# Performance work log

Hardware: AMD Instinct MI355X
Metric: run time of the kernel (lower is better)

## Reference

```python
import jax, jax.numpy as jnp
import numpy as np

NEG_SLOPE = 0.2


def setup_inputs() -> dict:
    key = jax.random.key(0)
    k1, k2, k3, k4 = jax.random.split(key, 4)
    N, E, IN, OUT = 100000, 1600000, 256, 64
    x = jax.random.normal(k1, (N, IN), dtype=jnp.float32)
    edge_index = jax.random.randint(k2, (2, E), 0, N, dtype=jnp.int64)
    W = jax.random.normal(k3, (IN, OUT), dtype=jnp.float32) * (1.0 / np.sqrt(IN))
    a = jax.random.normal(k4, (2 * OUT,), dtype=jnp.float32) * 0.02
    return {"x": x, "W": W, "a": a, "edge_index": edge_index, "num_nodes": N}


def reference(x, W, a, edge_index, num_nodes):
    # h = W(x): torch Linear without bias == x @ W (W stored as [in_dim, out_dim])
    h = x @ W                                   # [N, out_dim]
    src, dst = edge_index[0], edge_index[1]     # [E], [E]
    out_dim = h.shape[1]
    # e = LeakyReLU(cat([hs, hd]) @ a) == LeakyReLU(hs @ a[:d] + hd @ a[d:])
    s_src = h @ a[:out_dim]                     # [N] per-node src score
    s_dst = h @ a[out_dim:]                     # [N] per-node dst score
    e = jax.nn.leaky_relu(s_src[src] + s_dst[dst], NEG_SLOPE)  # [E]
    # per-destination segment softmax (numerically stable)
    m = jax.ops.segment_max(e, dst, num_segments=num_nodes)   # [N]
    ex = jnp.exp(e - m[dst])                                   # [E]
    denom = jax.ops.segment_sum(ex, dst, num_segments=num_nodes)  # [N]
    alpha = ex / denom[dst]                                    # [E]
    # weighted scatter-sum of source features into destinations
    out = jax.ops.segment_sum(h[src] * alpha[:, None], dst, num_segments=num_nodes)
    return out
```

## Files before the change

### kernel.cpp

```cpp
#include <hip/hip_runtime.h>
#include <hip/hip_bf16.h>
#include <math.h>

#define IN_DIM 256
#define OUT_DIM 64
#define NEG_SLOPE 0.2f
#define LCOLS 80
#define NBMAX 392
#define ECAP  10240
#define SENT  0xFFFFFFFFu
#define SCAP  2560

typedef __attribute__((ext_vector_type(8))) short bf16x8;
typedef __attribute__((ext_vector_type(4))) float f32x4;

static __device__ __forceinline__ ushort f2bf(float f) {
    union { __hip_bfloat16 b; ushort u; } cv;
    cv.b = __float2bfloat16(f);
    return cv.u;
}
static __device__ __forceinline__ float bf2f(ushort u) {
    union { ushort u2[2]; float f; } cv;
    cv.u2[0] = 0; cv.u2[1] = u;
    return cv.f;
}

__global__ __launch_bounds__(1024) void k0_fused(
        const float* __restrict__ W, const float* __restrict__ a,
        ushort* __restrict__ wb, int* __restrict__ gtail)
{
    __shared__ float wa_l[2 * IN_DIM];
    const int tid = threadIdx.x;

    if (tid < 512) gtail[tid] = 0;

    if (tid < IN_DIM) {
        const float* wr = W + (size_t)tid * OUT_DIM;
        float ss = 0.f, sd = 0.f;
        #pragma unroll
        for (int j = 0; j < OUT_DIM; ++j) {
            const float w = wr[j];
            ss = fmaf(w, a[j], ss);
            sd = fmaf(w, a[OUT_DIM + j], sd);
        }
        wa_l[tid] = ss;
        wa_l[IN_DIM + tid] = sd;
    }
    __syncthreads();

    for (int idx = tid; idx < 8 * 4 * LCOLS * 8; idx += 1024) {
        const int j   = idx & 7;
        const int col = (idx >> 3) % LCOLS;
        const int tk  = (idx >> 3) / LCOLS;
        const int k   = (tk >> 2) * 32 + (tk & 3) * 8 + j;
        float v = 0.f;
        if (col < OUT_DIM)           v = W[(size_t)k * OUT_DIM + col];
        else if (col == OUT_DIM)     v = wa_l[k];
        else if (col == OUT_DIM + 1) v = wa_l[IN_DIM + k];
        wb[idx] = f2bf(v);
    }
}

__global__ __launch_bounds__(256) void k1_mfma(
        const float* __restrict__ x, const ushort* __restrict__ wb,
        ushort* __restrict__ hb, float* __restrict__ s_src,
        float* __restrict__ s_dst, int N, int ngroups)
{
    __shared__ f32x4 red[5][4][64];

    const int tid  = threadIdx.x;
    const int wv   = tid >> 6;
    const int lane = tid & 63;
    const int l15  = lane & 15;
    const int khi  = lane >> 4;

    bf16x8 bfrag[2][5];
    #pragma unroll
    for (int tt = 0; tt < 2; ++tt) {
        const int t = 2 * wv + tt;
        #pragma unroll
        for (int c = 0; c < 5; ++c)
            bfrag[tt][c] =
                ((const bf16x8*)wb)[(t * 4 + khi) * LCOLS + c * 16 + l15];
    }

    for (int g = blockIdx.x; g < ngroups; g += gridDim.x) {
        const int row = min(g * 16 + l15, N - 1);
        const float* xp = x + (size_t)row * IN_DIM + wv * 64 + khi * 8;

        const float4 lo0 = *(const float4*)(xp);
        const float4 hi0 = *(const float4*)(xp + 4);
        const float4 lo1 = *(const float4*)(xp + 32);
        const float4 hi1 = *(const float4*)(xp + 36);

        union { bf16x8 v; ushort u[8]; } a0, a1;
        a0.u[0] = f2bf(lo0.x); a0.u[1] = f2bf(lo0.y);
        a0.u[2] = f2bf(lo0.z); a0.u[3] = f2bf(lo0.w);
        a0.u[4] = f2bf(hi0.x); a0.u[5] = f2bf(hi0.y);
        a0.u[6] = f2bf(hi0.z); a0.u[7] = f2bf(hi0.w);
        a1.u[0] = f2bf(lo1.x); a1.u[1] = f2bf(lo1.y);
        a1.u[2] = f2bf(lo1.z); a1.u[3] = f2bf(lo1.w);
        a1.u[4] = f2bf(hi1.x); a1.u[5] = f2bf(hi1.y);
        a1.u[6] = f2bf(hi1.z); a1.u[7] = f2bf(hi1.w);

        f32x4 acc[5] = {{0,0,0,0},{0,0,0,0},{0,0,0,0},{0,0,0,0},{0,0,0,0}};
        #pragma unroll
        for (int c = 0; c < 5; ++c)
            acc[c] = __builtin_amdgcn_mfma_f32_16x16x32_bf16(
                         a0.v, bfrag[0][c], acc[c], 0, 0, 0);
        #pragma unroll
        for (int c = 0; c < 5; ++c)
            acc[c] = __builtin_amdgcn_mfma_f32_16x16x32_bf16(
                         a1.v, bfrag[1][c], acc[c], 0, 0, 0);

        #pragma unroll
        for (int c = 0; c < 5; ++c)
            red[c][wv][lane] = acc[c];
        __syncthreads();

        f32x4 s = red[wv][0][lane];
        #pragma unroll
        for (int sw = 1; sw < 4; ++sw) s += red[wv][sw][lane];

        const int nrow0 = g * 16 + khi * 4;
        #pragma unroll
        for (int r = 0; r < 4; ++r) {
            const int nrow = nrow0 + r;
            if (nrow < N)
                hb[(size_t)nrow * OUT_DIM + wv * 16 + l15] = f2bf(s[r]);
        }

        if (wv == 0) {
            f32x4 s4 = red[4][0][lane];
            #pragma unroll
            for (int sw = 1; sw < 4; ++sw) s4 += red[4][sw][lane];
            #pragma unroll
            for (int r = 0; r < 4; ++r) {
                const int nrow = nrow0 + r;
                if (nrow < N) {
                    if (l15 == 0) s_src[nrow] = s4[r];
                    if (l15 == 1) s_dst[nrow] = s4[r];
                }
            }
        }
        __syncthreads();
    }
}

__global__ __launch_bounds__(256) void kA_bin(
        const int* __restrict__ ei, int* __restrict__ gtail,
        unsigned int* __restrict__ ebuf, int E, int nbuck)
{
    __shared__ unsigned int lbuf[NBMAX][32];
    __shared__ int lcnt[NBMAX];
    __shared__ int lfl[NBMAX];

    const int tid = threadIdx.x;
    for (int r = tid; r < nbuck; r += 256) { lcnt[r] = 0; lfl[r] = 0; }
    __syncthreads();

    const int e0 = (int)(((long long)blockIdx.x * E) / gridDim.x);
    const int e1 = (int)(((long long)(blockIdx.x + 1) * E) / gridDim.x);

    for (int b = e0; b < e1; b += 256) {
        const int i = b + tid;
        if (i < e1) {
            const unsigned int src = (unsigned int)ei[i];
            const int dst = ei[E + i];
            const int c = dst >> 8;
            const int pos = atomicAdd(&lcnt[c], 1);
            lbuf[c][pos & 31] = src | ((unsigned int)(dst & 255) << 17);
        }
        __syncthreads();
        for (int r = tid; r < nbuck; r += 256) {
            int cnt = lcnt[r];
            int fl  = lfl[r];
            while (cnt - fl >= 16) {
                const int gb = atomicAdd(&gtail[r], 16);
                if (gb + 16 <= ECAP) {
                    uint4* dp = (uint4*)(ebuf + (size_t)r * ECAP + gb);
                    const uint4* sp = (const uint4*)&lbuf[r][fl & 31];
                    dp[0] = sp[0]; dp[1] = sp[1]; dp[2] = sp[2]; dp[3] = sp[3];
                }
                fl += 16;
            }
            lfl[r] = fl;
        }
        __syncthreads();
    }

    for (int r = tid; r < nbuck; r += 256) {
        const int cnt = lcnt[r];
        const int fl  = lfl[r];
        if (cnt > fl) {
            const int gb = atomicAdd(&gtail[r], 16);
            if (gb + 16 <= ECAP) {
                unsigned int tmp[16];
                #pragma unroll
                for (int k = 0; k < 16; ++k)
                    tmp[k] = (fl + k < cnt) ? lbuf[r][(fl + k) & 31] : SENT;
                uint4* dp = (uint4*)(ebuf + (size_t)r * ECAP + gb);
                #pragma unroll
                for (int k = 0; k < 4; ++k)
                    dp[k] = make_uint4(tmp[4*k], tmp[4*k+1], tmp[4*k+2], tmp[4*k+3]);
            }
        }
    }
}

__global__ __launch_bounds__(256) void k2_bucket(
        const unsigned int* __restrict__ ebuf, const int* __restrict__ gtail,
        const ushort* __restrict__ hb, const float* __restrict__ s_src,
        const float* __restrict__ s_dst, float* __restrict__ out,
        int N, int nbuck)
{
    __shared__ int hist[64], bse[64], cur[64];
    __shared__ float sdl[64];
    __shared__ int2 spair[SCAP];

    const int bid = blockIdx.x;
    const int xcd = bid & 7;
    const int j8  = bid >> 3;
    const int H   = j8 & 3;
    const int B   = xcd + 8 * (j8 >> 2);
    if (B >= nbuck) return;

    const int tid = threadIdx.x;
    const int slots = min(gtail[B], ECAP);
    const unsigned int* eb = ebuf + (size_t)B * ECAP;
    const int dgb = B * 256 + H * 64;

    if (tid < 64) {
        hist[tid] = 0;
        const int dg = dgb + tid;
        sdl[tid] = (dg < N) ? s_dst[dg] : 0.f;
    }
    __syncthreads();

    for (int i = tid; i < slots; i += 256) {
        const unsigned int e = eb[i];
        if (e != SENT) {
            const int dl = (int)((e >> 17) & 255);
            if ((dl >> 6) == H) atomicAdd(&hist[dl & 63], 1);
        }
    }
    __syncthreads();

    if (tid < 64) {
        const int v = hist[tid];
        int s = v;
        #pragma unroll
        for (int off = 1; off < 64; off <<= 1) {
            const int u = __shfl_up(s, off, 64);
            if (tid >= off) s += u;
        }
        bse[tid] = s - v;
        cur[tid] = s - v;
    }
    __syncthreads();

    for (int i = tid; i < slots; i += 256) {
        const unsigned int e = eb[i];
        if (e != SENT) {
            const int dl = (int)((e >> 17) & 255);
            if ((dl >> 6) == H) {
                const int src = (int)(e & 0x1FFFF);
                const int d   = dl & 63;
                float sc = s_src[src] + sdl[d];
                sc = (sc > 0.f) ? sc : NEG_SLOPE * sc;
                const int pos = atomicAdd(&cur[d], 1);
                if (pos < SCAP)
                    spair[pos] = make_int2(src, __float_as_int(__expf(sc)));
            }
        }
    }
    __syncthreads();

    const int l15 = tid & 15;
    const int qw  = tid >> 4;
    #pragma unroll
    for (int k = 0; k < 4; ++k) {
        const int d  = qw + 16 * k;
        const int dg = dgb + d;
        if (dg >= N) continue;
        const int beg = bse[d];
        const int cnt = hist[d];
        const int je0 = min(beg, SCAP);
        const int je1 = min(beg + cnt, SCAP);
        const int m   = je1 - je0;

        float a0 = 0.f, a1 = 0.f, a2 = 0.f, a3 = 0.f, den = 0.f;
        #pragma unroll 4
        for (int j = 0; j < m; ++j) {
            const int2 p = spair[je0 + j];
            const float ex = __int_as_float(p.y);
            den += ex;
            const ushort4 hv = *(const ushort4*)(hb + ((size_t)p.x << 6) + (l15 << 2));
            a0 = fmaf(ex, bf2f(hv.x), a0);
            a1 = fmaf(ex, bf2f(hv.y), a1);
            a2 = fmaf(ex, bf2f(hv.z), a2);
            a3 = fmaf(ex, bf2f(hv.w), a3);
        }
        const float r = (m > 0) ? 1.f / den : 0.f;
        float4 v;
        v.x = a0 * r; v.y = a1 * r; v.z = a2 * r; v.w = a3 * r;
        *(float4*)(out + ((size_t)dg << 6) + (l15 << 2)) = v;
    }
}

extern "C" void kernel_launch(void* const* d_in, const int* in_sizes, int n_in,
                              void* d_out, int out_size, void* d_ws, size_t ws_size,
                              hipStream_t stream)
{
    const float* x  = (const float*)d_in[0];
    const float* W  = (const float*)d_in[1];
    const float* a  = (const float*)d_in[2];
    const int*   ei = (const int*)d_in[3];

    const int N = in_sizes[0] / IN_DIM;
    const int E = in_sizes[3] / 2;

    float* out = (float*)d_out;

    char* ws = (char*)d_ws;
    ushort* hb     = (ushort*)ws;                  ws += (size_t)N * OUT_DIM * 2;
    float*  s_src  = (float*)ws;                   ws += (size_t)N * 4;
    float*  s_dst  = (float*)ws;                   ws += (size_t)N * 4;
    ushort* wb     = (ushort*)ws;                  ws += 8 * 4 * LCOLS * 8 * 2;
    int*    gtail  = (int*)ws;                     ws += 512 * 4;
    unsigned int* ebuf = (unsigned int*)ws;        ws += (size_t)NBMAX * ECAP * 4;

    const int nbuck = (N + 255) >> 8;

    k0_fused<<<1, 1024, 0, stream>>>(W, a, wb, gtail);

    kA_bin<<<512, 256, 0, stream>>>(ei, gtail, ebuf, E, nbuck);

    const int ngroups = (N + 15) / 16;
    k1_mfma<<<1024, 256, 0, stream>>>(x, wb, hb, s_src, s_dst, N, ngroups);

    const int k2grid = 8 * 4 * ((nbuck + 7) / 8);
    k2_bucket<<<k2grid, 256, 0, stream>>>(ebuf, gtail, hb, s_src, s_dst, out, N, nbuck);
}
```

Baseline: 113.3 us.

## Merge edge binning and MFMA projection into one heterogeneous kernel launch

Combines the edge-binning kernel and the MFMA feature projection kernel into a single launch, with the first 512 blocks doing binning and the remaining 1024 blocks doing the matmul. The two phases are independent, so they can now run concurrently on the GPU and one launch plus its inter-kernel gap disappears. In exchange, every block reserves dynamic LDS sized for the larger binning buffer (about 53 KB), which may lower occupancy for the matmul blocks.

```diff
diff --git a/kernel.cpp b/kernel.cpp
--- a/kernel.cpp
+++ b/kernel.cpp
@@ -10,6 +10,8 @@
 #define ECAP  10240
 #define SENT  0xFFFFFFFFu
 #define SCAP  2560
+#define NBIN  512
+#define KAB_LDS (NBMAX * 32 * 4 + NBMAX * 4 + NBMAX * 4)
 
 typedef __attribute__((ext_vector_type(8))) short bf16x8;
 typedef __attribute__((ext_vector_type(4))) float f32x4;
@@ -61,149 +63,151 @@
     }
 }
 
-__global__ __launch_bounds__(256) void k1_mfma(
+__global__ __launch_bounds__(256) void kAB(
+        const int* __restrict__ ei, int* __restrict__ gtail,
+        unsigned int* __restrict__ ebuf, int E, int nbuck,
         const float* __restrict__ x, const ushort* __restrict__ wb,
         ushort* __restrict__ hb, float* __restrict__ s_src,
         float* __restrict__ s_dst, int N, int ngroups)
 {
-    __shared__ f32x4 red[5][4][64];
-
-    const int tid  = threadIdx.x;
-    const int wv   = tid >> 6;
-    const int lane = tid & 63;
-    const int l15  = lane & 15;
-    const int khi  = lane >> 4;
-
-    bf16x8 bfrag[2][5];
-    #pragma unroll
-    for (int tt = 0; tt < 2; ++tt) {
-        const int t = 2 * wv + tt;
+    extern __shared__ char smem[];
+    const int tid = threadIdx.x;
+
+    if (blockIdx.x < NBIN) {
+        unsigned int (*lbuf)[32] = (unsigned int(*)[32])smem;
+        int* lcnt = (int*)(smem + NBMAX * 32 * 4);
+        int* lfl  = lcnt + NBMAX;
+
+        for (int r = tid; r < nbuck; r += 256) { lcnt[r] = 0; lfl[r] = 0; }
+        __syncthreads();
+
+        const int e0 = (int)(((long long)blockIdx.x * E) / NBIN);
+        const int e1 = (int)(((long long)(blockIdx.x + 1) * E) / NBIN);
+
+        for (int b = e0; b < e1; b += 256) {
+            const int i = b + tid;
+            if (i < e1) {
+                const unsigned int src = (unsigned int)ei[i];
+                const int dst = ei[E + i];
+                const int c = dst >> 8;
+                const int pos = atomicAdd(&lcnt[c], 1);
+                lbuf[c][pos & 31] = src | ((unsigned int)(dst & 255) << 17);
+            }
+            __syncthreads();
+            for (int r = tid; r < nbuck; r += 256) {
+                int cnt = lcnt[r];
+                int fl  = lfl[r];
+                while (cnt - fl >= 16) {
+                    const int gb = atomicAdd(&gtail[r], 16);
+                    if (gb + 16 <= ECAP) {
+                        uint4* dp = (uint4*)(ebuf + (size_t)r * ECAP + gb);
+                        const uint4* sp = (const uint4*)&lbuf[r][fl & 31];
+                        dp[0] = sp[0]; dp[1] = sp[1]; dp[2] = sp[2]; dp[3] = sp[3];
+                    }
+                    fl += 16;
+                }
+                lfl[r] = fl;
+            }
+            __syncthreads();
+        }
+
+        for (int r = tid; r < nbuck; r += 256) {
+            const int cnt = lcnt[r];
+            const int fl  = lfl[r];
+            if (cnt > fl) {
+                const int gb = atomicAdd(&gtail[r], 16);
+                if (gb + 16 <= ECAP) {
+                    unsigned int tmp[16];
+                    #pragma unroll
+                    for (int k = 0; k < 16; ++k)
+                        tmp[k] = (fl + k < cnt) ? lbuf[r][(fl + k) & 31] : SENT;
+                    uint4* dp = (uint4*)(ebuf + (size_t)r * ECAP + gb);
+                    #pragma unroll
+                    for (int k = 0; k < 4; ++k)
+                        dp[k] = make_uint4(tmp[4*k], tmp[4*k+1],
+                                           tmp[4*k+2], tmp[4*k+3]);
+                }
+            }
+        }
+    } else {
+        f32x4 (*red)[4][64] = (f32x4(*)[4][64])smem;
+
+        const int wv   = tid >> 6;
+        const int lane = tid & 63;
+        const int l15  = lane & 15;
+        const int khi  = lane >> 4;
+
+        bf16x8 bfrag[2][5];
         #pragma unroll
-        for (int c = 0; c < 5; ++c)
-            bfrag[tt][c] =
-                ((const bf16x8*)wb)[(t * 4 + khi) * LCOLS + c * 16 + l15];
-    }
-
-    for (int g = blockIdx.x; g < ngroups; g += gridDim.x) {
-        const int row = min(g * 16 + l15, N - 1);
-        const float* xp = x + (size_t)row * IN_DIM + wv * 64 + khi * 8;
-
-        const float4 lo0 = *(const float4*)(xp);
-        const float4 hi0 = *(const float4*)(xp + 4);
-        const float4 lo1 = *(const float4*)(xp + 32);
-        const float4 hi1 = *(const float4*)(xp + 36);
-
-        union { bf16x8 v; ushort u[8]; } a0, a1;
-        a0.u[0] = f2bf(lo0.x); a0.u[1] = f2bf(lo0.y);
-        a0.u[2] = f2bf(lo0.z); a0.u[3] = f2bf(lo0.w);
-        a0.u[4] = f2bf(hi0.x); a0.u[5] = f2bf(hi0.y);
-        a0.u[6] = f2bf(hi0.z); a0.u[7] = f2bf(hi0.w);
-        a1.u[0] = f2bf(lo1.x); a1.u[1] = f2bf(lo1.y);
-        a1.u[2] = f2bf(lo1.z); a1.u[3] = f2bf(lo1.w);
-        a1.u[4] = f2bf(hi1.x); a1.u[5] = f2bf(hi1.y);
-        a1.u[6] = f2bf(hi1.z); a1.u[7] = f2bf(hi1.w);
-
-        f32x4 acc[5] = {{0,0,0,0},{0,0,0,0},{0,0,0,0},{0,0,0,0},{0,0,0,0}};
-        #pragma unroll
-        for (int c = 0; c < 5; ++c)
-            acc[c] = __builtin_amdgcn_mfma_f32_16x16x32_bf16(
-                         a0.v, bfrag[0][c], acc[c], 0, 0, 0);
-        #pragma unroll
-        for (int c = 0; c < 5; ++c)
-            acc[c] = __builtin_amdgcn_mfma_f32_16x16x32_bf16(
-                         a1.v, bfrag[1][c], acc[c], 0, 0, 0);
-
-        #pragma unroll
-        for (int c = 0; c < 5; ++c)
-            red[c][wv][lane] = acc[c];
-        __syncthreads();
-
-        f32x4 s = red[wv][0][lane];
-        #pragma unroll
-        for (int sw = 1; sw < 4; ++sw) s += red[wv][sw][lane];
-
-        const int nrow0 = g * 16 + khi * 4;
-        #pragma unroll
-        for (int r = 0; r < 4; ++r) {
-            const int nrow = nrow0 + r;
-            if (nrow < N)
-                hb[(size_t)nrow * OUT_DIM + wv * 16 + l15] = f2bf(s[r]);
-        }
-
-        if (wv == 0) {
-            f32x4 s4 = red[4][0][lane];
-            #pragma unroll
-            for (int sw = 1; sw < 4; ++sw) s4 += red[4][sw][lane];
+        for (int tt = 0; tt < 2; ++tt) {
+            const int t = 2 * wv + tt;
+            #pragma unroll
+            for (int c = 0; c < 5; ++c)
+                bfrag[tt][c] =
+                    ((const bf16x8*)wb)[(t * 4 + khi) * LCOLS + c * 16 + l15];
+        }
+
+        const int gstride = gridDim.x - NBIN;
+        for (int g = blockIdx.x - NBIN; g < ngroups; g += gstride) {
+            const int row = min(g * 16 + l15, N - 1);
+            const float* xp = x + (size_t)row * IN_DIM + wv * 64 + khi * 8;
+
+            const float4 lo0 = *(const float4*)(xp);
+            const float4 hi0 = *(const float4*)(xp + 4);
+            const float4 lo1 = *(const float4*)(xp + 32);
+            const float4 hi1 = *(const float4*)(xp + 36);
+
+            union { bf16x8 v; ushort u[8]; } a0, a1;
+            a0.u[0] = f2bf(lo0.x); a0.u[1] = f2bf(lo0.y);
+            a0.u[2] = f2bf(lo0.z); a0.u[3] = f2bf(lo0.w);
+            a0.u[4] = f2bf(hi0.x); a0.u[5] = f2bf(hi0.y);
+            a0.u[6] = f2bf(hi0.z); a0.u[7] = f2bf(hi0.w);
+            a1.u[0] = f2bf(lo1.x); a1.u[1] = f2bf(lo1.y);
+            a1.u[2] = f2bf(lo1.z); a1.u[3] = f2bf(lo1.w);
+            a1.u[4] = f2bf(hi1.x); a1.u[5] = f2bf(hi1.y);
+            a1.u[6] = f2bf(hi1.z); a1.u[7] = f2bf(hi1.w);
+
+            f32x4 acc[5] = {{0,0,0,0},{0,0,0,0},{0,0,0,0},{0,0,0,0},{0,0,0,0}};
+            #pragma unroll
+            for (int c = 0; c < 5; ++c)
+                acc[c] = __builtin_amdgcn_mfma_f32_16x16x32_bf16(
+                             a0.v, bfrag[0][c], acc[c], 0, 0, 0);
+            #pragma unroll
+            for (int c = 0; c < 5; ++c)
+                acc[c] = __builtin_amdgcn_mfma_f32_16x16x32_bf16(
+                             a1.v, bfrag[1][c], acc[c], 0, 0, 0);
+
+            #pragma unroll
+            for (int c = 0; c < 5; ++c)
+                red[c][wv][lane] = acc[c];
+            __syncthreads();
+
+            f32x4 s = red[wv][0][lane];
+            #pragma unroll
+            for (int sw = 1; sw < 4; ++sw) s += red[wv][sw][lane];
+
+            const int nrow0 = g * 16 + khi * 4;
             #pragma unroll
             for (int r = 0; r < 4; ++r) {
                 const int nrow = nrow0 + r;
-                if (nrow < N) {
-                    if (l15 == 0) s_src[nrow] = s4[r];
-                    if (l15 == 1) s_dst[nrow] = s4[r];
+                if (nrow < N)
+                    hb[(size_t)nrow * OUT_DIM + wv * 16 + l15] = f2bf(s[r]);
+            }
+
+            if (wv == 0) {
+                f32x4 s4 = red[4][0][lane];
+                #pragma unroll
+                for (int sw = 1; sw < 4; ++sw) s4 += red[4][sw][lane];
+                #pragma unroll
+                for (int r = 0; r < 4; ++r) {
+                    const int nrow = nrow0 + r;
+                    if (nrow < N) {
+                        if (l15 == 0) s_src[nrow] = s4[r];
+                        if (l15 == 1) s_dst[nrow] = s4[r];
+                    }
                 }
             }
-        }
-        __syncthreads();
-    }
-}
-
-__global__ __launch_bounds__(256) void kA_bin(
-        const int* __restrict__ ei, int* __restrict__ gtail,
-        unsigned int* __restrict__ ebuf, int E, int nbuck)
-{
-    __shared__ unsigned int lbuf[NBMAX][32];
-    __shared__ int lcnt[NBMAX];
-    __shared__ int lfl[NBMAX];
-
-    const int tid = threadIdx.x;
-    for (int r = tid; r < nbuck; r += 256) { lcnt[r] = 0; lfl[r] = 0; }
-    __syncthreads();
-
-    const int e0 = (int)(((long long)blockIdx.x * E) / gridDim.x);
-    const int e1 = (int)(((long long)(blockIdx.x + 1) * E) / gridDim.x);
-
-    for (int b = e0; b < e1; b += 256) {
-        const int i = b + tid;
-        if (i < e1) {
-            const unsigned int src = (unsigned int)ei[i];
-            const int dst = ei[E + i];
-            const int c = dst >> 8;
-            const int pos = atomicAdd(&lcnt[c], 1);
-            lbuf[c][pos & 31] = src | ((unsigned int)(dst & 255) << 17);
-        }
-        __syncthreads();
-        for (int r = tid; r < nbuck; r += 256) {
-            int cnt = lcnt[r];
-            int fl  = lfl[r];
-            while (cnt - fl >= 16) {
-                const int gb = atomicAdd(&gtail[r], 16);
-                if (gb + 16 <= ECAP) {
-                    uint4* dp = (uint4*)(ebuf + (size_t)r * ECAP + gb);
-                    const uint4* sp = (const uint4*)&lbuf[r][fl & 31];
-                    dp[0] = sp[0]; dp[1] = sp[1]; dp[2] = sp[2]; dp[3] = sp[3];
-                }
-                fl += 16;
-            }
-            lfl[r] = fl;
-        }
-        __syncthreads();
-    }
-
-    for (int r = tid; r < nbuck; r += 256) {
-        const int cnt = lcnt[r];
-        const int fl  = lfl[r];
-        if (cnt > fl) {
-            const int gb = atomicAdd(&gtail[r], 16);
-            if (gb + 16 <= ECAP) {
-                unsigned int tmp[16];
-                #pragma unroll
-                for (int k = 0; k < 16; ++k)
-                    tmp[k] = (fl + k < cnt) ? lbuf[r][(fl + k) & 31] : SENT;
-                uint4* dp = (uint4*)(ebuf + (size_t)r * ECAP + gb);
-                #pragma unroll
-                for (int k = 0; k < 4; ++k)
-                    dp[k] = make_uint4(tmp[4*k], tmp[4*k+1], tmp[4*k+2], tmp[4*k+3]);
-            }
+            __syncthreads();
         }
     }
 }
@@ -334,10 +338,9 @@
 
     k0_fused<<<1, 1024, 0, stream>>>(W, a, wb, gtail);
 
-    kA_bin<<<512, 256, 0, stream>>>(ei, gtail, ebuf, E, nbuck);
-
     const int ngroups = (N + 15) / 16;
-    k1_mfma<<<1024, 256, 0, stream>>>(x, wb, hb, s_src, s_dst, N, ngroups);
+    kAB<<<NBIN + 1024, 256, KAB_LDS, stream>>>(ei, gtail, ebuf, E, nbuck,
+                                               x, wb, hb, s_src, s_dst, N, ngroups);
 
     const int k2grid = 8 * 4 * ((nbuck + 7) / 8);
     k2_bucket<<<k2grid, 256, 0, stream>>>(ebuf, gtail, hb, s_src, s_dst, out, N, nbuck);
```

Result: faster. 108.9 us (-3.9%).
